# Kernel tuning notes

Measured on AMD Instinct MI355X. Metric: run time of the kernel, lower is better.

The kernel has to match this reference:

```python
import jax, jax.numpy as jnp
import numpy as np

N = 50000
EPS = 1e-5
SLOPE = 0.1


def gcn_conv(x, edge_index, W, b):
    # add self loops
    loops = jnp.arange(N, dtype=edge_index.dtype)
    row = jnp.concatenate([edge_index[0], loops])
    col = jnp.concatenate([edge_index[1], loops])
    x = x @ W + b  # [N, out]
    deg = jax.ops.segment_sum(jnp.ones_like(col, dtype=x.dtype), col, num_segments=N)
    dinv = jnp.where(deg > 0, deg ** -0.5, 0.0)
    norm = dinv[row] * dinv[col]  # [E+N]
    msg = norm[:, None] * x[row]  # edge-sized intermediate
    return jax.ops.segment_sum(msg, col, num_segments=N)


def batchnorm(x, gamma, beta):
    # training-mode BatchNorm1d over node dim, biased variance
    mu = jnp.mean(x, axis=0)
    var = jnp.mean((x - mu) ** 2, axis=0)
    return (x - mu) * jax.lax.rsqrt(var + EPS) * gamma + beta


def leaky_relu(x):
    return jnp.where(x >= 0, x, SLOPE * x)


def setup_inputs() -> dict:
    key = jax.random.key(0)
    ks = jax.random.split(key, 6)
    x = jax.random.normal(ks[0], (N, 256), dtype=jnp.float32)
    edge_index = jax.random.randint(ks[1], (2, 600000), 0, N, dtype=jnp.int64)
    W1 = jax.random.normal(ks[2], (256, 128), dtype=jnp.float32) * (1.0 / np.sqrt(256))
    b1 = jnp.zeros((128,), dtype=jnp.float32)
    W2 = jax.random.normal(ks[3], (128, 128), dtype=jnp.float32) * (1.0 / np.sqrt(128))
    b2 = jnp.zeros((128,), dtype=jnp.float32)
    g1 = jnp.ones((128,), dtype=jnp.float32)
    be1 = jnp.zeros((128,), dtype=jnp.float32)
    g2 = jnp.ones((128,), dtype=jnp.float32)
    be2 = jnp.zeros((128,), dtype=jnp.float32)
    return {"x": x, "edge_index": edge_index, "W1": W1, "b1": b1, "W2": W2, "b2": b2,
            "g1": g1, "be1": be1, "g2": g2, "be2": be2}


def reference(x, edge_index, W1, b1, W2, b2, g1, be1, g2, be2):
    h = gcn_conv(x, edge_index, W1, b1)
    h = leaky_relu(batchnorm(h, g1, be1))
    h = gcn_conv(h, edge_index, W2, b2)
    h = leaky_relu(batchnorm(h, g2, be2))
    return h
```

## Files before the change

### kernel.cpp

```cpp
#include <hip/hip_runtime.h>

#define NODES 50000
#define FIN   256
#define FOUT  128
#define EPS   1e-5f
#define SLOPE 0.1f
#define SCAN_CHUNK 512
#define SCAN_NB ((NODES + SCAN_CHUNK - 1) / SCAN_CHUNK)

typedef __attribute__((ext_vector_type(8))) short short8_t;
typedef __attribute__((ext_vector_type(4))) float f32x4_t;

__device__ __forceinline__ ushort f2bf(float f) {
    union { float f; unsigned u; } v; v.f = f;
    return (ushort)((v.u + 0x7FFFu + ((v.u >> 16) & 1u)) >> 16);
}
__device__ __forceinline__ float bf2f(ushort u) {
    union { unsigned x; float f; } v; v.x = ((unsigned)u) << 16; return v.f;
}

__global__ void deg_kernel(const int* __restrict__ col, int E, int* __restrict__ deg) {
    int e = blockIdx.x * 256 + threadIdx.x;
    if (e < E) atomicAdd(&deg[col[e]], 1);
}

__global__ __launch_bounds__(256) void scan1_kernel(const int* __restrict__ deg,
                                                    int* __restrict__ partials, int Nn) {
    const int t = threadIdx.x;
    const int i0 = blockIdx.x * SCAN_CHUNK + 2 * t;
    int e0 = (i0 < Nn) ? deg[i0] : 0;
    int e1 = (i0 + 1 < Nn) ? deg[i0 + 1] : 0;
    __shared__ int sh[256];
    sh[t] = e0 + e1;
    __syncthreads();
    for (int off = 128; off > 0; off >>= 1) {
        if (t < off) sh[t] += sh[t + off];
        __syncthreads();
    }
    if (t == 0) partials[blockIdx.x] = sh[0];
}

__global__ __launch_bounds__(128) void scan2_kernel(const int* __restrict__ partials,
                                                    int* __restrict__ partials_pre,
                                                    int* __restrict__ offN, int total) {
    __shared__ int sh[128];
    const int t = threadIdx.x;
    int v = (t < SCAN_NB) ? partials[t] : 0;
    sh[t] = v;
    __syncthreads();
    for (int off = 1; off < 128; off <<= 1) {
        int u = (t >= off) ? sh[t - off] : 0;
        __syncthreads();
        sh[t] += u;
        __syncthreads();
    }
    if (t < SCAN_NB) partials_pre[t] = sh[t] - v;
    if (t == 0) *offN = total;
}

__global__ __launch_bounds__(256) void scan3_kernel(const int* __restrict__ deg,
                                                    const int* __restrict__ partials_pre,
                                                    int* __restrict__ offsets,
                                                    float* __restrict__ dinv, int Nn) {
    const int t = threadIdx.x;
    const int i0 = blockIdx.x * SCAN_CHUNK + 2 * t;
    int e0 = (i0 < Nn) ? deg[i0] : 0;
    int e1 = (i0 + 1 < Nn) ? deg[i0 + 1] : 0;
    int s = e0 + e1;
    __shared__ int sh[256];
    sh[t] = s;
    __syncthreads();
    for (int off = 1; off < 256; off <<= 1) {
        int u = (t >= off) ? sh[t - off] : 0;
        __syncthreads();
        sh[t] += u;
        __syncthreads();
    }
    int ex = sh[t] - s + partials_pre[blockIdx.x];
    if (i0 < Nn)     { offsets[i0] = ex;          dinv[i0] = rsqrtf((float)(e0 + 1)); }
    if (i0 + 1 < Nn) { offsets[i0 + 1] = ex + e0; dinv[i0 + 1] = rsqrtf((float)(e1 + 1)); }
}

__global__ void fill_kernel(const int* __restrict__ row, const int* __restrict__ col, int E,
                            const int* __restrict__ offsets, int* __restrict__ cursor,
                            int* __restrict__ srcs) {
    int e = blockIdx.x * 256 + threadIdx.x;
    if (e < E) {
        int c = col[e];
        int p = offsets[c] + atomicAdd(&cursor[c], 1);
        srcs[p] = row[e];
    }
}

template <int K>
__global__ __launch_bounds__(256) void wcvt_kernel(const float* __restrict__ W,
                                                   ushort* __restrict__ Bt) {
    int idx = blockIdx.x * 256 + threadIdx.x;
    int k = idx >> 7, n = idx & 127;
    if (k < K) Bt[n * K + k] = f2bf(W[idx]);
}

__global__ void bn_finalize_kernel(const float* __restrict__ sum, const float* __restrict__ sumsq,
                                   const float* __restrict__ gamma, const float* __restrict__ beta,
                                   float* __restrict__ scale, float* __restrict__ shift) {
    int f = threadIdx.x;
    const float invN = 1.0f / (float)NODES;
    float mu  = sum[f] * invN;
    float var = sumsq[f] * invN - mu * mu;
    float sc  = gamma[f] * rsqrtf(var + EPS);
    scale[f] = sc;
    shift[f] = beta[f] - mu * sc;
}

template <int K, bool FUSE>
__global__ __launch_bounds__(256) void gemm_mfma_kernel(const float* __restrict__ A,
                                                        const ushort* __restrict__ Bt,
                                                        const float* __restrict__ bias,
                                                        const float* __restrict__ scale,
                                                        const float* __restrict__ shift,
                                                        ushort* __restrict__ C, int M) {
    __shared__ ushort As[128 * 40];
    __shared__ ushort Bs[128 * 40];
    const int tid  = threadIdx.x;
    const int lane = tid & 63;
    const int w    = tid >> 6;
    const int m0   = blockIdx.x * 128;
    const int ml   = lane & 15;
    const int kg   = lane >> 4;

    f32x4_t acc[2][8];
    const f32x4_t zero = {0.f, 0.f, 0.f, 0.f};
#pragma unroll
    for (int a = 0; a < 2; ++a)
#pragma unroll
        for (int b = 0; b < 8; ++b) acc[a][b] = zero;

    const int sr = tid >> 1;
    const int sh = tid & 1;
    const bool aok = (m0 + sr) < M;
    const float* ap = A + (size_t)(m0 + sr) * K + sh * 16;

    for (int k0 = 0; k0 < K; k0 += 32) {
        __syncthreads();
        float vv[16];
        if (aok) {
            const float* p = ap + k0;
            *(float4*)&vv[0]  = *(const float4*)(p + 0);
            *(float4*)&vv[4]  = *(const float4*)(p + 4);
            *(float4*)&vv[8]  = *(const float4*)(p + 8);
            *(float4*)&vv[12] = *(const float4*)(p + 12);
            if (FUSE) {
                int kb = k0 + sh * 16;
#pragma unroll
                for (int j = 0; j < 16; ++j) {
                    float val = fmaf(vv[j], scale[kb + j], shift[kb + j]);
                    vv[j] = (val >= 0.f) ? val : SLOPE * val;
                }
            }
        } else {
#pragma unroll
            for (int j = 0; j < 16; ++j) vv[j] = 0.f;
        }
        short8_t oa, ob;
#pragma unroll
        for (int j = 0; j < 8; ++j) { oa[j] = (short)f2bf(vv[j]); ob[j] = (short)f2bf(vv[8 + j]); }
        *(short8_t*)&As[sr * 40 + sh * 16]     = oa;
        *(short8_t*)&As[sr * 40 + sh * 16 + 8] = ob;
#pragma unroll
        for (int cc = 0; cc < 2; ++cc) {
            int c  = tid + cc * 256;
            int bn = c >> 2;
            int bs = (c & 3) * 8;
            *(short8_t*)&Bs[bn * 40 + bs] = *(const short8_t*)&Bt[bn * K + k0 + bs];
        }
        __syncthreads();
        short8_t af0 = *(const short8_t*)&As[(w * 32 + ml) * 40 + kg * 8];
        short8_t af1 = *(const short8_t*)&As[(w * 32 + 16 + ml) * 40 + kg * 8];
#pragma unroll
        for (int nt = 0; nt < 8; ++nt) {
            short8_t bf = *(const short8_t*)&Bs[(nt * 16 + ml) * 40 + kg * 8];
            acc[0][nt] = __builtin_amdgcn_mfma_f32_16x16x32_bf16(af0, bf, acc[0][nt], 0, 0, 0);
            acc[1][nt] = __builtin_amdgcn_mfma_f32_16x16x32_bf16(af1, bf, acc[1][nt], 0, 0, 0);
        }
    }
#pragma unroll
    for (int nt = 0; nt < 8; ++nt) {
        float bv = bias[nt * 16 + ml];
#pragma unroll
        for (int mt = 0; mt < 2; ++mt) {
            int mr0 = m0 + w * 32 + mt * 16 + kg * 4;
#pragma unroll
            for (int rr = 0; rr < 4; ++rr) {
                int mr = mr0 + rr;
                if (mr < M) C[(size_t)mr * FOUT + nt * 16 + ml] = f2bf(acc[mt][nt][rr] + bv);
            }
        }
    }
}

__global__ __launch_bounds__(256) void agg_kernel(const ushort* __restrict__ h,
                                                  const float* __restrict__ dinv,
                                                  const int* __restrict__ offsets,
                                                  const int* __restrict__ srcs,
                                                  float* __restrict__ out, int Nn) {
    const int sub  = threadIdx.x >> 5;
    const int lane = threadIdx.x & 31;
    int node = blockIdx.x * 8 + sub;
    if (node >= Nn) return;
    const ushort4* __restrict__ h4 = (const ushort4*)h;
    float di = dinv[node];
    ushort4 hv = h4[(size_t)node * 32 + lane];
    float sw = di * di;
    float4 a0, a1, a2, a3;
    a0.x = sw * bf2f(hv.x); a0.y = sw * bf2f(hv.y);
    a0.z = sw * bf2f(hv.z); a0.w = sw * bf2f(hv.w);
    a1 = make_float4(0.f, 0.f, 0.f, 0.f);
    a2 = a1;
    a3 = a1;
    int beg = offsets[node], end = offsets[node + 1];
    int e = beg;
    for (; e + 4 <= end; e += 4) {
        int i0 = srcs[e], i1 = srcs[e + 1], i2 = srcs[e + 2], i3 = srcs[e + 3];
        float n0 = di * dinv[i0], n1 = di * dinv[i1];
        float n2 = di * dinv[i2], n3 = di * dinv[i3];
        ushort4 v0 = h4[(size_t)i0 * 32 + lane];
        ushort4 v1 = h4[(size_t)i1 * 32 + lane];
        ushort4 v2 = h4[(size_t)i2 * 32 + lane];
        ushort4 v3 = h4[(size_t)i3 * 32 + lane];
        a0.x = fmaf(n0, bf2f(v0.x), a0.x); a0.y = fmaf(n0, bf2f(v0.y), a0.y);
        a0.z = fmaf(n0, bf2f(v0.z), a0.z); a0.w = fmaf(n0, bf2f(v0.w), a0.w);
        a1.x = fmaf(n1, bf2f(v1.x), a1.x); a1.y = fmaf(n1, bf2f(v1.y), a1.y);
        a1.z = fmaf(n1, bf2f(v1.z), a1.z); a1.w = fmaf(n1, bf2f(v1.w), a1.w);
        a2.x = fmaf(n2, bf2f(v2.x), a2.x); a2.y = fmaf(n2, bf2f(v2.y), a2.y);
        a2.z = fmaf(n2, bf2f(v2.z), a2.z); a2.w = fmaf(n2, bf2f(v2.w), a2.w);
        a3.x = fmaf(n3, bf2f(v3.x), a3.x); a3.y = fmaf(n3, bf2f(v3.y), a3.y);
        a3.z = fmaf(n3, bf2f(v3.z), a3.z); a3.w = fmaf(n3, bf2f(v3.w), a3.w);
    }
    for (; e < end; ++e) {
        int s = srcs[e];
        float n = di * dinv[s];
        ushort4 v = h4[(size_t)s * 32 + lane];
        a0.x = fmaf(n, bf2f(v.x), a0.x); a0.y = fmaf(n, bf2f(v.y), a0.y);
        a0.z = fmaf(n, bf2f(v.z), a0.z); a0.w = fmaf(n, bf2f(v.w), a0.w);
    }
    a0.x += a1.x + a2.x + a3.x;
    a0.y += a1.y + a2.y + a3.y;
    a0.z += a1.z + a2.z + a3.z;
    a0.w += a1.w + a2.w + a3.w;
    float4* __restrict__ o4 = (float4*)out;
    o4[(size_t)node * 32 + lane] = a0;
}

__global__ __launch_bounds__(256) void bn_stats_kernel(const float* __restrict__ x,
                                                       float* __restrict__ sum,
                                                       float* __restrict__ sumsq, int Nn) {
    const int T = gridDim.x * 256;
    int tid = blockIdx.x * 256 + threadIdx.x;
    float s1 = 0.f, s2 = 0.f;
    for (size_t i = tid; i < (size_t)Nn * FOUT; i += T) {
        float v = x[i];
        s1 += v;
        s2 += v * v;
    }
    __shared__ float sh1[256], sh2[256];
    sh1[threadIdx.x] = s1;
    sh2[threadIdx.x] = s2;
    __syncthreads();
    if (threadIdx.x < 128) {
        s1 = sh1[threadIdx.x] + sh1[threadIdx.x + 128];
        s2 = sh2[threadIdx.x] + sh2[threadIdx.x + 128];
        int f = (blockIdx.x * 256 + threadIdx.x) & 127;
        atomicAdd(&sum[f], s1);
        atomicAdd(&sumsq[f], s2);
    }
}

__global__ __launch_bounds__(256) void bn_apply_kernel(float* __restrict__ x,
                                                       const float* __restrict__ sum,
                                                       const float* __restrict__ sumsq,
                                                       const float* __restrict__ gamma,
                                                       const float* __restrict__ beta, int Nn) {
    size_t i = (size_t)blockIdx.x * 256 + threadIdx.x;
    if (i >= (size_t)Nn * FOUT) return;
    int f = (int)(i & 127);
    const float invN = 1.0f / (float)NODES;
    float mu  = sum[f] * invN;
    float var = sumsq[f] * invN - mu * mu;
    float sc  = gamma[f] * rsqrtf(var + EPS);
    float v   = (x[i] - mu) * sc + beta[f];
    x[i] = (v >= 0.f) ? v : SLOPE * v;
}

extern "C" void kernel_launch(void* const* d_in, const int* in_sizes, int n_in,
                              void* d_out, int out_size, void* d_ws, size_t ws_size,
                              hipStream_t stream) {
    const float* x  = (const float*)d_in[0];
    const int*   ei = (const int*)d_in[1];
    const float* W1 = (const float*)d_in[2];
    const float* b1 = (const float*)d_in[3];
    const float* W2 = (const float*)d_in[4];
    const float* b2 = (const float*)d_in[5];
    const float* g1 = (const float*)d_in[6];
    const float* be1 = (const float*)d_in[7];
    const float* g2 = (const float*)d_in[8];
    const float* be2 = (const float*)d_in[9];
    float* out = (float*)d_out;

    const int E = in_sizes[1] / 2;
    const int* erow = ei;
    const int* ecol = ei + E;

    ushort* bufA    = (ushort*)d_ws;
    float* dinv     = (float*)d_ws + (size_t)NODES * FOUT;
    int*   deg      = (int*)(dinv + NODES);
    int*   cursor   = deg + NODES;
    float* colsumA  = (float*)(cursor + NODES);
    float* colsqA   = colsumA + 128;
    float* colsumB  = colsqA + 128;
    float* colsqB   = colsumB + 128;
    int*   offsets  = (int*)(colsqB + 128);
    int*   srcs     = offsets + (NODES + 1);
    int*   partials = srcs + E;
    int*   partpre  = partials + SCAN_NB;
    float* scaleA   = (float*)d_ws + 3300000;
    float* shiftA   = scaleA + 128;
    ushort* Bt1 = (ushort*)cursor;
    ushort* Bt2 = Bt1 + 128 * FIN;

    size_t zero_bytes = (size_t)(2 * NODES) * sizeof(int) + 4 * 128 * sizeof(float);
    hipMemsetAsync(deg, 0, zero_bytes, stream);

    int egrid = (E + 255) / 256;
    deg_kernel<<<egrid, 256, 0, stream>>>(ecol, E, deg);
    scan1_kernel<<<SCAN_NB, 256, 0, stream>>>(deg, partials, NODES);
    scan2_kernel<<<1, 128, 0, stream>>>(partials, partpre, &offsets[NODES], E);
    scan3_kernel<<<SCAN_NB, 256, 0, stream>>>(deg, partpre, offsets, dinv, NODES);
    fill_kernel<<<egrid, 256, 0, stream>>>(erow, ecol, E, offsets, cursor, srcs);
    wcvt_kernel<FIN><<<(128 * FIN) / 256, 256, 0, stream>>>(W1, Bt1);
    wcvt_kernel<FOUT><<<(128 * FOUT) / 256, 256, 0, stream>>>(W2, Bt2);

    const int mg = (NODES + 127) / 128;
    const int ag = (NODES + 7) / 8;
    const int eg = ((size_t)NODES * FOUT + 255) / 256;

    gemm_mfma_kernel<FIN, false><<<mg, 256, 0, stream>>>(x, Bt1, b1, nullptr, nullptr, bufA, NODES);
    agg_kernel<<<ag, 256, 0, stream>>>(bufA, dinv, offsets, srcs, out, NODES);
    bn_stats_kernel<<<256, 256, 0, stream>>>(out, colsumA, colsqA, NODES);
    bn_finalize_kernel<<<1, 128, 0, stream>>>(colsumA, colsqA, g1, be1, scaleA, shiftA);

    gemm_mfma_kernel<FOUT, true><<<mg, 256, 0, stream>>>(out, Bt2, b2, scaleA, shiftA, bufA, NODES);
    agg_kernel<<<ag, 256, 0, stream>>>(bufA, dinv, offsets, srcs, out, NODES);
    bn_stats_kernel<<<256, 256, 0, stream>>>(out, colsumB, colsqB, NODES);
    bn_apply_kernel<<<eg, 256, 0, stream>>>(out, colsumB, colsqB, g2, be2, NODES);
}
```

Before: 340.0 us.

## Fuse BatchNorm statistics into aggregation kernel with per-block partial sums

The aggregation kernel now also accumulates per-feature sum and sum-of-squares while writing outputs. It runs as a fixed grid-stride grid with 16 lanes per node and 16-byte loads, and writes per-block partials that a single 1024-thread kernel reduces into scale and shift. This removes the separate bn_stats pass, which re-read the whole 50000x128 float output, along with its float atomics. bn_apply now takes precomputed scale and shift. The cost is fewer threads per node in the gather, and a single-block reduction over 2048 partials that runs serially on the stream.

```diff
diff --git a/kernel.cpp b/kernel.cpp
--- a/kernel.cpp
+++ b/kernel.cpp
@@ -7,6 +7,7 @@
 #define SLOPE 0.1f
 #define SCAN_CHUNK 512
 #define SCAN_NB ((NODES + SCAN_CHUNK - 1) / SCAN_CHUNK)
+#define AGG_NB 2048
 
 typedef __attribute__((ext_vector_type(8))) short short8_t;
 typedef __attribute__((ext_vector_type(4))) float f32x4_t;
@@ -100,16 +101,34 @@
     if (k < K) Bt[n * K + k] = f2bf(W[idx]);
 }
 
-__global__ void bn_finalize_kernel(const float* __restrict__ sum, const float* __restrict__ sumsq,
-                                   const float* __restrict__ gamma, const float* __restrict__ beta,
-                                   float* __restrict__ scale, float* __restrict__ shift) {
-    int f = threadIdx.x;
-    const float invN = 1.0f / (float)NODES;
-    float mu  = sum[f] * invN;
-    float var = sumsq[f] * invN - mu * mu;
-    float sc  = gamma[f] * rsqrtf(var + EPS);
-    scale[f] = sc;
-    shift[f] = beta[f] - mu * sc;
+__global__ __launch_bounds__(1024) void bn_reduce_kernel(const float* __restrict__ ps1,
+                                                         const float* __restrict__ ps2,
+                                                         const float* __restrict__ gamma,
+                                                         const float* __restrict__ beta,
+                                                         float* __restrict__ scale,
+                                                         float* __restrict__ shift) {
+    const int f = threadIdx.x & 127;
+    const int c = threadIdx.x >> 7;
+    float s1 = 0.f, s2 = 0.f;
+    for (int b = c; b < AGG_NB; b += 8) {
+        s1 += ps1[b * 128 + f];
+        s2 += ps2[b * 128 + f];
+    }
+    __shared__ float r1[8][128], r2[8][128];
+    r1[c][f] = s1;
+    r2[c][f] = s2;
+    __syncthreads();
+    if (threadIdx.x < 128) {
+        float t1 = 0.f, t2 = 0.f;
+#pragma unroll
+        for (int k = 0; k < 8; ++k) { t1 += r1[k][f]; t2 += r2[k][f]; }
+        const float invN = 1.0f / (float)NODES;
+        float mu  = t1 * invN;
+        float var = t2 * invN - mu * mu;
+        float sc  = gamma[f] * rsqrtf(var + EPS);
+        scale[f] = sc;
+        shift[f] = beta[f] - mu * sc;
+    }
 }
 
 template <int K, bool FUSE>
@@ -202,92 +221,93 @@
                                                   const float* __restrict__ dinv,
                                                   const int* __restrict__ offsets,
                                                   const int* __restrict__ srcs,
-                                                  float* __restrict__ out, int Nn) {
-    const int sub  = threadIdx.x >> 5;
-    const int lane = threadIdx.x & 31;
-    int node = blockIdx.x * 8 + sub;
-    if (node >= Nn) return;
-    const ushort4* __restrict__ h4 = (const ushort4*)h;
-    float di = dinv[node];
-    ushort4 hv = h4[(size_t)node * 32 + lane];
-    float sw = di * di;
-    float4 a0, a1, a2, a3;
-    a0.x = sw * bf2f(hv.x); a0.y = sw * bf2f(hv.y);
-    a0.z = sw * bf2f(hv.z); a0.w = sw * bf2f(hv.w);
-    a1 = make_float4(0.f, 0.f, 0.f, 0.f);
-    a2 = a1;
-    a3 = a1;
-    int beg = offsets[node], end = offsets[node + 1];
-    int e = beg;
-    for (; e + 4 <= end; e += 4) {
-        int i0 = srcs[e], i1 = srcs[e + 1], i2 = srcs[e + 2], i3 = srcs[e + 3];
-        float n0 = di * dinv[i0], n1 = di * dinv[i1];
-        float n2 = di * dinv[i2], n3 = di * dinv[i3];
-        ushort4 v0 = h4[(size_t)i0 * 32 + lane];
-        ushort4 v1 = h4[(size_t)i1 * 32 + lane];
-        ushort4 v2 = h4[(size_t)i2 * 32 + lane];
-        ushort4 v3 = h4[(size_t)i3 * 32 + lane];
-        a0.x = fmaf(n0, bf2f(v0.x), a0.x); a0.y = fmaf(n0, bf2f(v0.y), a0.y);
-        a0.z = fmaf(n0, bf2f(v0.z), a0.z); a0.w = fmaf(n0, bf2f(v0.w), a0.w);
-        a1.x = fmaf(n1, bf2f(v1.x), a1.x); a1.y = fmaf(n1, bf2f(v1.y), a1.y);
-        a1.z = fmaf(n1, bf2f(v1.z), a1.z); a1.w = fmaf(n1, bf2f(v1.w), a1.w);
-        a2.x = fmaf(n2, bf2f(v2.x), a2.x); a2.y = fmaf(n2, bf2f(v2.y), a2.y);
-        a2.z = fmaf(n2, bf2f(v2.z), a2.z); a2.w = fmaf(n2, bf2f(v2.w), a2.w);
-        a3.x = fmaf(n3, bf2f(v3.x), a3.x); a3.y = fmaf(n3, bf2f(v3.y), a3.y);
-        a3.z = fmaf(n3, bf2f(v3.z), a3.z); a3.w = fmaf(n3, bf2f(v3.w), a3.w);
-    }
-    for (; e < end; ++e) {
-        int s = srcs[e];
-        float n = di * dinv[s];
-        ushort4 v = h4[(size_t)s * 32 + lane];
-        a0.x = fmaf(n, bf2f(v.x), a0.x); a0.y = fmaf(n, bf2f(v.y), a0.y);
-        a0.z = fmaf(n, bf2f(v.z), a0.z); a0.w = fmaf(n, bf2f(v.w), a0.w);
-    }
-    a0.x += a1.x + a2.x + a3.x;
-    a0.y += a1.y + a2.y + a3.y;
-    a0.z += a1.z + a2.z + a3.z;
-    a0.w += a1.w + a2.w + a3.w;
-    float4* __restrict__ o4 = (float4*)out;
-    o4[(size_t)node * 32 + lane] = a0;
-}
-
-__global__ __launch_bounds__(256) void bn_stats_kernel(const float* __restrict__ x,
-                                                       float* __restrict__ sum,
-                                                       float* __restrict__ sumsq, int Nn) {
-    const int T = gridDim.x * 256;
-    int tid = blockIdx.x * 256 + threadIdx.x;
-    float s1 = 0.f, s2 = 0.f;
-    for (size_t i = tid; i < (size_t)Nn * FOUT; i += T) {
-        float v = x[i];
-        s1 += v;
-        s2 += v * v;
-    }
-    __shared__ float sh1[256], sh2[256];
-    sh1[threadIdx.x] = s1;
-    sh2[threadIdx.x] = s2;
-    __syncthreads();
-    if (threadIdx.x < 128) {
-        s1 = sh1[threadIdx.x] + sh1[threadIdx.x + 128];
-        s2 = sh2[threadIdx.x] + sh2[threadIdx.x + 128];
-        int f = (blockIdx.x * 256 + threadIdx.x) & 127;
-        atomicAdd(&sum[f], s1);
-        atomicAdd(&sumsq[f], s2);
+                                                  float* __restrict__ out,
+                                                  float* __restrict__ ps1,
+                                                  float* __restrict__ ps2, int Nn) {
+    const int tid  = threadIdx.x;
+    const int g    = tid >> 4;
+    const int lane = tid & 15;
+    float s1[8], s2[8];
+#pragma unroll
+    for (int j = 0; j < 8; ++j) { s1[j] = 0.f; s2[j] = 0.f; }
+
+    for (int node = blockIdx.x * 16 + g; node < Nn; node += AGG_NB * 16) {
+        float di = dinv[node];
+        short8_t hv = *(const short8_t*)&h[(size_t)node * 128 + lane * 8];
+        float sw = di * di;
+        float a0[8], a1[8];
+#pragma unroll
+        for (int j = 0; j < 8; ++j) { a0[j] = sw * bf2f((ushort)hv[j]); a1[j] = 0.f; }
+        int beg = offsets[node], end = offsets[node + 1];
+        int e = beg;
+        for (; e + 4 <= end; e += 4) {
+            int i0 = srcs[e], i1 = srcs[e + 1], i2 = srcs[e + 2], i3 = srcs[e + 3];
+            float n0 = di * dinv[i0], n1 = di * dinv[i1];
+            float n2 = di * dinv[i2], n3 = di * dinv[i3];
+            short8_t v0 = *(const short8_t*)&h[(size_t)i0 * 128 + lane * 8];
+            short8_t v1 = *(const short8_t*)&h[(size_t)i1 * 128 + lane * 8];
+            short8_t v2 = *(const short8_t*)&h[(size_t)i2 * 128 + lane * 8];
+            short8_t v3 = *(const short8_t*)&h[(size_t)i3 * 128 + lane * 8];
+#pragma unroll
+            for (int j = 0; j < 8; ++j) {
+                a0[j] = fmaf(n0, bf2f((ushort)v0[j]), a0[j]);
+                a1[j] = fmaf(n1, bf2f((ushort)v1[j]), a1[j]);
+                a0[j] = fmaf(n2, bf2f((ushort)v2[j]), a0[j]);
+                a1[j] = fmaf(n3, bf2f((ushort)v3[j]), a1[j]);
+            }
+        }
+        for (; e < end; ++e) {
+            int s = srcs[e];
+            float n = di * dinv[s];
+            short8_t v = *(const short8_t*)&h[(size_t)s * 128 + lane * 8];
+#pragma unroll
+            for (int j = 0; j < 8; ++j) a0[j] = fmaf(n, bf2f((ushort)v[j]), a0[j]);
+        }
+        float4 o0, o1;
+        o0.x = a0[0] + a1[0]; o0.y = a0[1] + a1[1];
+        o0.z = a0[2] + a1[2]; o0.w = a0[3] + a1[3];
+        o1.x = a0[4] + a1[4]; o1.y = a0[5] + a1[5];
+        o1.z = a0[6] + a1[6]; o1.w = a0[7] + a1[7];
+        float* op = &out[(size_t)node * 128 + lane * 8];
+        *(float4*)op       = o0;
+        *(float4*)(op + 4) = o1;
+        s1[0] += o0.x; s2[0] += o0.x * o0.x;  s1[1] += o0.y; s2[1] += o0.y * o0.y;
+        s1[2] += o0.z; s2[2] += o0.z * o0.z;  s1[3] += o0.w; s2[3] += o0.w * o0.w;
+        s1[4] += o1.x; s2[4] += o1.x * o1.x;  s1[5] += o1.y; s2[5] += o1.y * o1.y;
+        s1[6] += o1.z; s2[6] += o1.z * o1.z;  s1[7] += o1.w; s2[7] += o1.w * o1.w;
+    }
+
+    __shared__ float red[256][8];
+#pragma unroll
+    for (int j = 0; j < 8; ++j) red[tid][j] = s1[j];
+    __syncthreads();
+    if (tid < 128) {
+        int ln = tid >> 3, jj = tid & 7;
+        float s = 0.f;
+#pragma unroll
+        for (int gg = 0; gg < 16; ++gg) s += red[gg * 16 + ln][jj];
+        ps1[blockIdx.x * 128 + tid] = s;
+    }
+    __syncthreads();
+#pragma unroll
+    for (int j = 0; j < 8; ++j) red[tid][j] = s2[j];
+    __syncthreads();
+    if (tid < 128) {
+        int ln = tid >> 3, jj = tid & 7;
+        float s = 0.f;
+#pragma unroll
+        for (int gg = 0; gg < 16; ++gg) s += red[gg * 16 + ln][jj];
+        ps2[blockIdx.x * 128 + tid] = s;
     }
 }
 
 __global__ __launch_bounds__(256) void bn_apply_kernel(float* __restrict__ x,
-                                                       const float* __restrict__ sum,
-                                                       const float* __restrict__ sumsq,
-                                                       const float* __restrict__ gamma,
-                                                       const float* __restrict__ beta, int Nn) {
+                                                       const float* __restrict__ scale,
+                                                       const float* __restrict__ shift, int Nn) {
     size_t i = (size_t)blockIdx.x * 256 + threadIdx.x;
     if (i >= (size_t)Nn * FOUT) return;
     int f = (int)(i & 127);
-    const float invN = 1.0f / (float)NODES;
-    float mu  = sum[f] * invN;
-    float var = sumsq[f] * invN - mu * mu;
-    float sc  = gamma[f] * rsqrtf(var + EPS);
-    float v   = (x[i] - mu) * sc + beta[f];
+    float v = fmaf(x[i], scale[f], shift[f]);
     x[i] = (v >= 0.f) ? v : SLOPE * v;
 }
 
@@ -314,20 +334,20 @@
     float* dinv     = (float*)d_ws + (size_t)NODES * FOUT;
     int*   deg      = (int*)(dinv + NODES);
     int*   cursor   = deg + NODES;
-    float* colsumA  = (float*)(cursor + NODES);
-    float* colsqA   = colsumA + 128;
-    float* colsumB  = colsqA + 128;
-    float* colsqB   = colsumB + 128;
-    int*   offsets  = (int*)(colsqB + 128);
+    float* scaleA   = (float*)(cursor + NODES);
+    float* shiftA   = scaleA + 128;
+    float* scaleB   = shiftA + 128;
+    float* shiftB   = scaleB + 128;
+    int*   offsets  = (int*)(shiftB + 128);
     int*   srcs     = offsets + (NODES + 1);
     int*   partials = srcs + E;
     int*   partpre  = partials + SCAN_NB;
-    float* scaleA   = (float*)d_ws + 3300000;
-    float* shiftA   = scaleA + 128;
+    float* ps1      = (float*)(partpre + SCAN_NB);
+    float* ps2      = ps1 + AGG_NB * 128;
     ushort* Bt1 = (ushort*)cursor;
     ushort* Bt2 = Bt1 + 128 * FIN;
 
-    size_t zero_bytes = (size_t)(2 * NODES) * sizeof(int) + 4 * 128 * sizeof(float);
+    size_t zero_bytes = (size_t)(2 * NODES) * sizeof(int);
     hipMemsetAsync(deg, 0, zero_bytes, stream);
 
     int egrid = (E + 255) / 256;
@@ -340,16 +360,14 @@
     wcvt_kernel<FOUT><<<(128 * FOUT) / 256, 256, 0, stream>>>(W2, Bt2);
 
     const int mg = (NODES + 127) / 128;
-    const int ag = (NODES + 7) / 8;
     const int eg = ((size_t)NODES * FOUT + 255) / 256;
 
     gemm_mfma_kernel<FIN, false><<<mg, 256, 0, stream>>>(x, Bt1, b1, nullptr, nullptr, bufA, NODES);
-    agg_kernel<<<ag, 256, 0, stream>>>(bufA, dinv, offsets, srcs, out, NODES);
-    bn_stats_kernel<<<256, 256, 0, stream>>>(out, colsumA, colsqA, NODES);
-    bn_finalize_kernel<<<1, 128, 0, stream>>>(colsumA, colsqA, g1, be1, scaleA, shiftA);
+    agg_kernel<<<AGG_NB, 256, 0, stream>>>(bufA, dinv, offsets, srcs, out, ps1, ps2, NODES);
+    bn_reduce_kernel<<<1, 1024, 0, stream>>>(ps1, ps2, g1, be1, scaleA, shiftA);
 
     gemm_mfma_kernel<FOUT, true><<<mg, 256, 0, stream>>>(out, Bt2, b2, scaleA, shiftA, bufA, NODES);
-    agg_kernel<<<ag, 256, 0, stream>>>(bufA, dinv, offsets, srcs, out, NODES);
-    bn_stats_kernel<<<256, 256, 0, stream>>>(out, colsumB, colsqB, NODES);
-    bn_apply_kernel<<<eg, 256, 0, stream>>>(out, colsumB, colsqB, g2, be2, NODES);
-}
+    agg_kernel<<<AGG_NB, 256, 0, stream>>>(bufA, dinv, offsets, srcs, out, ps1, ps2, NODES);
+    bn_reduce_kernel<<<1, 1024, 0, stream>>>(ps1, ps2, g2, be2, scaleB, shiftB);
+    bn_apply_kernel<<<eg, 256, 0, stream>>>(out, scaleB, shiftB, NODES);
+}
```

Result: slower. 437.7 us (+28.7%).
